# Performance work log

Hardware: AMD Instinct MI355X
Metric: run time of the kernel (lower is better)

The kernel has to match this reference:

```python
import jax, jax.numpy as jnp
import numpy as np

N = 100000      # nodes
E = 1600000     # edges (before self-loops)
IN = 128        # input feature dim
HID = 64        # hidden channels per head
H = 4           # heads in layer 1
OUT = 2         # output classes
NEG_SLOPE = 0.2 # GATConv LeakyReLU slope


def setup_inputs() -> dict:
    key = jax.random.key(0)
    ks = jax.random.split(key, 10)
    x = jax.random.normal(ks[0], (N, IN), jnp.float32)
    edge_index = jax.random.randint(ks[1], (2, E), 0, N)
    W1 = jax.random.normal(ks[2], (IN, H * HID), jnp.float32) / np.sqrt(IN).astype(np.float32)
    a1_src = jax.random.normal(ks[3], (H, HID), jnp.float32) * 0.1
    a1_dst = jax.random.normal(ks[4], (H, HID), jnp.float32) * 0.1
    b1 = jnp.zeros((H * HID,), jnp.float32)
    W2 = jax.random.normal(ks[5], (H * HID, OUT), jnp.float32) / np.sqrt(H * HID).astype(np.float32)
    a2_src = jax.random.normal(ks[6], (1, OUT), jnp.float32) * 0.1
    a2_dst = jax.random.normal(ks[7], (1, OUT), jnp.float32) * 0.1
    b2 = jnp.zeros((OUT,), jnp.float32)
    return {"x": x, "edge_index": edge_index, "W1": W1, "a1_src": a1_src,
            "a1_dst": a1_dst, "b1": b1, "W2": W2, "a2_src": a2_src,
            "a2_dst": a2_dst, "b2": b2}


def gat_layer(x, src, dst, W, a_s, a_d, bias, heads, ch):
    """PyG GATConv (concat=True): gather -> LeakyReLU score -> segment softmax -> scatter-add."""
    n = x.shape[0]
    h = (x @ W).reshape(n, heads, ch)                     # [N, H, C]
    s_src = (h * a_s).sum(-1)                             # [N, H]
    s_dst = (h * a_d).sum(-1)                             # [N, H]
    e = jax.nn.leaky_relu(s_src[src] + s_dst[dst], NEG_SLOPE)  # [E, H]
    m = jax.ops.segment_max(e, dst, num_segments=n)       # per-dst max for stability
    m = jnp.where(jnp.isfinite(m), m, 0.0)
    ex = jnp.exp(e - m[dst])
    denom = jax.ops.segment_sum(ex, dst, num_segments=n)
    alpha = ex / denom[dst]                               # [E, H]
    out = jax.ops.segment_sum(alpha[..., None] * h[src], dst, num_segments=n)  # [N, H, C]
    return out.reshape(n, heads * ch) + bias


def reference(x, edge_index, W1, a1_src, a1_dst, b1, W2, a2_src, a2_dst, b2):
    loops = jnp.arange(N, dtype=edge_index.dtype)         # GATConv adds self-loops
    src = jnp.concatenate([edge_index[0], loops])
    dst = jnp.concatenate([edge_index[1], loops])
    h = jax.nn.elu(gat_layer(x, src, dst, W1, a1_src, a1_dst, b1, H, HID))
    return gat_layer(h, src, dst, W2, a2_src, a2_dst, b2, 1, OUT)
```

## Files before the change

### kernel.cpp

```cpp
#include <hip/hip_runtime.h>
#include <hip/hip_bf16.h>
#include <hip/hip_fp16.h>

#define NN    100000
#define EE    1600000
#define ETOT  1700000
#define IN_D  128
#define C1    256
#define NHEAD 4
#define HID   64
#define OUTD  2
#define SLOPE 0.2f
#define SLOTS 64
#define BB    8
#define NBKT  196
#define BCAP  12288

#define BKT_BLOCKS  ((ETOT + 256 * BB - 1) / (256 * BB))
#define CONV_BLOCKS 128
#define CSR_BLOCKS  NBKT
#define GEMM_BLOCKS (NN / 16)

typedef _Float16 f16x8 __attribute__((ext_vector_type(8)));
typedef float f32x4 __attribute__((ext_vector_type(4)));

__device__ __forceinline__ float lrelu(float x) {
    return x > 0.0f ? x : SLOPE * x;
}

struct alignas(8) h4 { __half2 a, b; };

__global__ __launch_bounds__(256) void bucket_and_convert(
    const int* __restrict__ ei, const float* __restrict__ W1,
    int* __restrict__ gcnt, int2* __restrict__ buf, _Float16* __restrict__ W1T)
{
    if (blockIdx.x >= BKT_BLOCKS) {
        int idx = (blockIdx.x - BKT_BLOCKS) * 256 + threadIdx.x;
        int k = idx >> 8;
        int c = idx & 255;
        W1T[c * IN_D + k] = (_Float16)W1[idx];
        return;
    }

    __shared__ int hist[NBKT], curb[NBKT], gbase[NBKT];
    const int t = threadIdx.x;
    for (int i = t; i < NBKT; i += 256) { hist[i] = 0; curb[i] = 0; }
    __syncthreads();

    const int base = blockIdx.x * 256 * BB;
    int srcs[BB], dsts[BB];
#pragma unroll
    for (int i = 0; i < BB; i++) {
        const int e = base + i * 256 + t;
        int s = -1, d = -1;
        if (e < ETOT) {
            if (e < EE) { s = ei[e]; d = ei[EE + e]; }
            else        { s = d = e - EE; }
        }
        srcs[i] = s; dsts[i] = d;
        if (d >= 0) atomicAdd(&hist[d >> 9], 1);
    }
    __syncthreads();
    for (int i = t; i < NBKT; i += 256)
        if (hist[i] > 0) gbase[i] = atomicAdd(&gcnt[i], hist[i]);
    __syncthreads();
#pragma unroll
    for (int i = 0; i < BB; i++) {
        if (dsts[i] >= 0) {
            int b = dsts[i] >> 9;
            int slot = atomicAdd(&curb[b], 1);
            int pos = gbase[b] + slot;
            if (pos < BCAP) buf[b * BCAP + pos] = make_int2(srcs[i], dsts[i]);
        }
    }
}

__global__ __launch_bounds__(256) void csr_and_gemm(
    const int* __restrict__ gcnt, const int2* __restrict__ buf,
    int* __restrict__ deg, int* __restrict__ csr,
    const float* __restrict__ x, const _Float16* __restrict__ W1T,
    const float* __restrict__ a1s, const float* __restrict__ a1d,
    __half* __restrict__ hh1, float* __restrict__ s1s, float* __restrict__ s1d)
{
    __shared__ int cur[512];
    __shared__ _Float16 xl[16][136];

    if (blockIdx.x < CSR_BLOCKS) {
        const int t = threadIdx.x;
        const int b = blockIdx.x;
        cur[t] = 0; cur[t + 256] = 0;
        __syncthreads();
        const int cnt = min(gcnt[b], BCAP);
        const int2* bp = buf + b * BCAP;
        for (int i = t; i < cnt; i += 256) {
            int2 p = bp[i];
            int slot = atomicAdd(&cur[p.y & 511], 1);
            if (slot < SLOTS) csr[p.y * SLOTS + slot] = p.x;
        }
        __syncthreads();
        const int n0 = b * 512;
        if (n0 + t < NN)       deg[n0 + t]       = min(cur[t], SLOTS);
        if (n0 + 256 + t < NN) deg[n0 + 256 + t] = min(cur[t + 256], SLOTS);
        return;
    }

    const int tid = threadIdx.x;
    const int n0 = (blockIdx.x - CSR_BLOCKS) * 16;
    {
        const int row = tid >> 4;
        const int col = (tid & 15) * 8;
        const float4* xs = (const float4*)(x + (long)(n0 + row) * IN_D + col);
        float4 v0 = xs[0], v1 = xs[1];
        f16x8 hv;
        hv[0] = (_Float16)v0.x; hv[1] = (_Float16)v0.y;
        hv[2] = (_Float16)v0.z; hv[3] = (_Float16)v0.w;
        hv[4] = (_Float16)v1.x; hv[5] = (_Float16)v1.y;
        hv[6] = (_Float16)v1.z; hv[7] = (_Float16)v1.w;
        *(f16x8*)&xl[row][col] = hv;
    }
    __syncthreads();

    const int lane = tid & 63;
    const int w = tid >> 6;
    const int nd = lane & 15;
    const int g = lane >> 4;

    f16x8 bfrag[4];
#pragma unroll
    for (int ks = 0; ks < 4; ks++)
        bfrag[ks] = *(const f16x8*)&xl[nd][ks * 32 + g * 8];

    f32x4 acc[4] = {{0.f,0.f,0.f,0.f},{0.f,0.f,0.f,0.f},
                    {0.f,0.f,0.f,0.f},{0.f,0.f,0.f,0.f}};
#pragma unroll
    for (int t = 0; t < 4; t++) {
        const _Float16* wbase = W1T + (64 * w + 16 * t + nd) * IN_D + g * 8;
#pragma unroll
        for (int ks = 0; ks < 4; ks++) {
            f16x8 afrag = *(const f16x8*)(wbase + ks * 32);
            acc[t] = __builtin_amdgcn_mfma_f32_16x16x32_f16(
                afrag, bfrag[ks], acc[t], 0, 0, 0);
        }
    }

    float vs = 0.f, vd = 0.f;
#pragma unroll
    for (int t = 0; t < 4; t++) {
        const int cbase = 64 * w + 16 * t + 4 * g;
        const float4 as4 = *(const float4*)(a1s + cbase);
        const float4 ad4 = *(const float4*)(a1d + cbase);
        vs += acc[t][0] * as4.x + acc[t][1] * as4.y
            + acc[t][2] * as4.z + acc[t][3] * as4.w;
        vd += acc[t][0] * ad4.x + acc[t][1] * ad4.y
            + acc[t][2] * ad4.z + acc[t][3] * ad4.w;
        h4 hv;
        hv.a = __floats2half2_rn(acc[t][0], acc[t][1]);
        hv.b = __floats2half2_rn(acc[t][2], acc[t][3]);
        *(h4*)&hh1[(long)(n0 + nd) * C1 + cbase] = hv;
    }
    vs += __shfl_xor(vs, 16); vs += __shfl_xor(vs, 32);
    vd += __shfl_xor(vd, 16); vd += __shfl_xor(vd, 32);
    if (lane < 16) {
        s1s[(n0 + lane) * NHEAD + w] = vs;
        s1d[(n0 + lane) * NHEAD + w] = vd;
    }
}

__global__ __launch_bounds__(256) void l1_fused(
    const int* __restrict__ csr, const int* __restrict__ deg,
    const float* __restrict__ s1s, const float* __restrict__ s1d,
    const __half* __restrict__ hh1, const float* __restrict__ b1,
    const float* __restrict__ W2, const float* __restrict__ a2s,
    const float* __restrict__ a2d, float4* __restrict__ nrec)
{
    const int lane = threadIdx.x & 63;
    const int wid = threadIdx.x >> 6;
    const int n = blockIdx.x * 4 + wid;
    if (n >= NN) return;

    const int eid = lane & 15;
    const int h = lane >> 4;
    const int hsel = lane & 48;
    const int dn = deg[n];
    const int st = n * SLOTS;

    const float4 sdv = ((const float4*)s1d)[n];
    const float sdh = (h == 0) ? sdv.x : (h == 1) ? sdv.y
                    : (h == 2) ? sdv.z : sdv.w;

    float a0 = 0.f, a1 = 0.f, a2 = 0.f, a3 = 0.f, dl = 0.f;

    const int nch = (dn + 15) >> 4;
    for (int c = 0; c < nch; ++c) {
        const int idx = c * 16 + eid;
        const int eidx = idx < dn ? idx : dn - 1;
        int sc = csr[st + eidx];
        float ssh = s1s[sc * 4 + h];
        float w = (idx < dn) ? __expf(lrelu(ssh + sdh)) : 0.f;
#pragma unroll
        for (int j = 0; j < 16; ++j) {
            int sj = __builtin_amdgcn_readlane(sc, j);
            float wv = __shfl(w, hsel | j);
            const h4* rowp = (const h4*)(hh1 + (long)sj * C1);
            h4 hv = rowp[lane];
            float2 f01 = __half22float2(hv.a);
            float2 f23 = __half22float2(hv.b);
            dl += wv;
            a0 = fmaf(wv, f01.x, a0);
            a1 = fmaf(wv, f01.y, a1);
            a2 = fmaf(wv, f23.x, a2);
            a3 = fmaf(wv, f23.y, a3);
        }
    }

    const float4 bv = ((const float4*)b1)[lane];
    float v0 = a0 / dl + bv.x;
    float v1 = a1 / dl + bv.y;
    float v2 = a2 / dl + bv.z;
    float v3 = a3 / dl + bv.w;
    v0 = v0 > 0.f ? v0 : expm1f(v0);
    v1 = v1 > 0.f ? v1 : expm1f(v1);
    v2 = v2 > 0.f ? v2 : expm1f(v2);
    v3 = v3 > 0.f ? v3 : expm1f(v3);

    const float4 wa = ((const float4*)W2)[lane * 2];
    const float4 wb = ((const float4*)W2)[lane * 2 + 1];
    float p0 = v0 * wa.x + v1 * wa.z + v2 * wb.x + v3 * wb.z;
    float p1 = v0 * wa.y + v1 * wa.w + v2 * wb.y + v3 * wb.w;
#pragma unroll
    for (int off = 32; off >= 1; off >>= 1) {
        p0 += __shfl_xor(p0, off);
        p1 += __shfl_xor(p1, off);
    }
    if (lane == 0) {
        nrec[n] = make_float4(p0, p1,
                              p0 * a2s[0] + p1 * a2s[1],
                              p0 * a2d[0] + p1 * a2d[1]);
    }
}

__global__ __launch_bounds__(256) void l2_fused(
    const int* __restrict__ csr, const int* __restrict__ deg,
    const float4* __restrict__ nrec, const float* __restrict__ b2,
    float* __restrict__ out)
{
    const int sl = threadIdx.x & 15;
    const int grp = threadIdx.x >> 4;
    const int n = blockIdx.x * 16 + grp;
    if (n >= NN) return;

    const int dn = deg[n];
    const float sd = nrec[n].w;
    float den = 0.f, a0 = 0.f, a1 = 0.f;
    for (int slot = sl; slot < dn; slot += 16) {
        int s = csr[n * SLOTS + slot];
        float4 r = nrec[s];
        float w = __expf(lrelu(r.z + sd));
        den += w;
        a0 = fmaf(w, r.x, a0);
        a1 = fmaf(w, r.y, a1);
    }
#pragma unroll
    for (int off = 8; off >= 1; off >>= 1) {
        den += __shfl_xor(den, off);
        a0  += __shfl_xor(a0, off);
        a1  += __shfl_xor(a1, off);
    }
    if (sl == 0) {
        out[n * 2]     = a0 / den + b2[0];
        out[n * 2 + 1] = a1 / den + b2[1];
    }
}

extern "C" void kernel_launch(void* const* d_in, const int* in_sizes, int n_in,
                              void* d_out, int out_size, void* d_ws, size_t ws_size,
                              hipStream_t stream) {
    const float* x   = (const float*)d_in[0];
    const int*   ei  = (const int*)d_in[1];
    const float* W1  = (const float*)d_in[2];
    const float* a1s = (const float*)d_in[3];
    const float* a1d = (const float*)d_in[4];
    const float* b1  = (const float*)d_in[5];
    const float* W2  = (const float*)d_in[6];
    const float* a2s = (const float*)d_in[7];
    const float* a2d = (const float*)d_in[8];
    const float* b2  = (const float*)d_in[9];
    float* out = (float*)d_out;

    float* ws = (float*)d_ws;
    __half* hh1 = (__half*)ws;
    float* s1s = ws + (long)NN * C1 / 2;
    float* s1d = s1s + NN * NHEAD;
    float4* nrec = (float4*)(s1d + NN * NHEAD);
    int* deg  = (int*)(nrec + NN);
    int* csr  = deg + NN;
    _Float16* W1T = (_Float16*)(csr + (long)NN * SLOTS);
    int* gcnt = (int*)(W1T + C1 * IN_D);
    int2* buf = (int2*)(gcnt + 256);

    hipMemsetAsync(gcnt, 0, 256 * sizeof(int), stream);

    bucket_and_convert<<<BKT_BLOCKS + CONV_BLOCKS, 256, 0, stream>>>(
        ei, W1, gcnt, buf, W1T);
    csr_and_gemm<<<CSR_BLOCKS + GEMM_BLOCKS, 256, 0, stream>>>(
        gcnt, buf, deg, csr, x, W1T, a1s, a1d, hh1, s1s, s1d);
    l1_fused<<<(NN + 3) / 4, 256, 0, stream>>>(csr, deg, s1s, s1d, hh1,
                                               b1, W2, a2s, a2d, nrec);
    l2_fused<<<(NN + 15) / 16, 256, 0, stream>>>(csr, deg, nrec, b2, out);
}
```

Before: 253.7 us.

## Pack bucketed edges into 32-bit words and split CSR build across two blocks

Bucket entries now hold the local destination index (9 bits) and source (17 bits) packed into one int instead of an int2, which halves the bucket buffer writes and reads. The CSR build uses two blocks per bucket, each taking nodes of one parity, so more blocks run and the shared-memory counters shrink. Each of those blocks still reads the whole bucket, so total buffer reads are unchanged from before. The l1 gather now indexes the half rows with 32-bit arithmetic (sj<<6) rather than a long multiply.

```diff
diff --git a/kernel.cpp b/kernel.cpp
--- a/kernel.cpp
+++ b/kernel.cpp
@@ -18,7 +18,7 @@
 
 #define BKT_BLOCKS  ((ETOT + 256 * BB - 1) / (256 * BB))
 #define CONV_BLOCKS 128
-#define CSR_BLOCKS  NBKT
+#define CSR_BLOCKS  (2 * NBKT)
 #define GEMM_BLOCKS (NN / 16)
 
 typedef _Float16 f16x8 __attribute__((ext_vector_type(8)));
@@ -32,7 +32,7 @@
 
 __global__ __launch_bounds__(256) void bucket_and_convert(
     const int* __restrict__ ei, const float* __restrict__ W1,
-    int* __restrict__ gcnt, int2* __restrict__ buf, _Float16* __restrict__ W1T)
+    int* __restrict__ gcnt, int* __restrict__ buf, _Float16* __restrict__ W1T)
 {
     if (blockIdx.x >= BKT_BLOCKS) {
         int idx = (blockIdx.x - BKT_BLOCKS) * 256 + threadIdx.x;
@@ -70,37 +70,41 @@
             int b = dsts[i] >> 9;
             int slot = atomicAdd(&curb[b], 1);
             int pos = gbase[b] + slot;
-            if (pos < BCAP) buf[b * BCAP + pos] = make_int2(srcs[i], dsts[i]);
+            if (pos < BCAP) buf[b * BCAP + pos] = ((dsts[i] & 511) << 17) | srcs[i];
         }
     }
 }
 
 __global__ __launch_bounds__(256) void csr_and_gemm(
-    const int* __restrict__ gcnt, const int2* __restrict__ buf,
+    const int* __restrict__ gcnt, const int* __restrict__ buf,
     int* __restrict__ deg, int* __restrict__ csr,
     const float* __restrict__ x, const _Float16* __restrict__ W1T,
     const float* __restrict__ a1s, const float* __restrict__ a1d,
     __half* __restrict__ hh1, float* __restrict__ s1s, float* __restrict__ s1d)
 {
-    __shared__ int cur[512];
+    __shared__ int cur[256];
     __shared__ _Float16 xl[16][136];
 
     if (blockIdx.x < CSR_BLOCKS) {
         const int t = threadIdx.x;
-        const int b = blockIdx.x;
-        cur[t] = 0; cur[t + 256] = 0;
+        const int b = blockIdx.x >> 1;
+        const int par = blockIdx.x & 1;
+        cur[t] = 0;
         __syncthreads();
         const int cnt = min(gcnt[b], BCAP);
-        const int2* bp = buf + b * BCAP;
+        const int* bp = buf + b * BCAP;
+        const int n0 = b * 512;
         for (int i = t; i < cnt; i += 256) {
-            int2 p = bp[i];
-            int slot = atomicAdd(&cur[p.y & 511], 1);
-            if (slot < SLOTS) csr[p.y * SLOTS + slot] = p.x;
+            int v = bp[i];
+            int dl = v >> 17;
+            if ((dl & 1) == par) {
+                int slot = atomicAdd(&cur[dl >> 1], 1);
+                if (slot < SLOTS) csr[(n0 + dl) * SLOTS + slot] = v & 0x1FFFF;
+            }
         }
         __syncthreads();
-        const int n0 = b * 512;
-        if (n0 + t < NN)       deg[n0 + t]       = min(cur[t], SLOTS);
-        if (n0 + 256 + t < NN) deg[n0 + 256 + t] = min(cur[t + 256], SLOTS);
+        const int n = n0 + 2 * t + par;
+        if (n < NN) deg[n] = min(cur[t], SLOTS);
         return;
     }
 
@@ -183,6 +187,7 @@
     const int hsel = lane & 48;
     const int dn = deg[n];
     const int st = n * SLOTS;
+    const h4* __restrict__ hb = (const h4*)hh1;
 
     const float4 sdv = ((const float4*)s1d)[n];
     const float sdh = (h == 0) ? sdv.x : (h == 1) ? sdv.y
@@ -201,8 +206,7 @@
         for (int j = 0; j < 16; ++j) {
             int sj = __builtin_amdgcn_readlane(sc, j);
             float wv = __shfl(w, hsel | j);
-            const h4* rowp = (const h4*)(hh1 + (long)sj * C1);
-            h4 hv = rowp[lane];
+            h4 hv = hb[(sj << 6) + lane];
             float2 f01 = __half22float2(hv.a);
             float2 f23 = __half22float2(hv.b);
             dl += wv;
@@ -296,7 +300,7 @@
     int* csr  = deg + NN;
     _Float16* W1T = (_Float16*)(csr + (long)NN * SLOTS);
     int* gcnt = (int*)(W1T + C1 * IN_D);
-    int2* buf = (int2*)(gcnt + 256);
+    int* buf = gcnt + 256;
 
     hipMemsetAsync(gcnt, 0, 256 * sizeof(int), stream);
 
```

After: 249.8 us. Within noise of the previous version (-1.5%).
